# Performance work log

Measured on AMD Instinct MI355X. Metric: run time of the kernel, lower is better.

Reference implementation:

```python
import jax, jax.numpy as jnp
import numpy as np

MAX_DISP = 200


def conv2d(x, w, b):
    # x: [N,C,H,W], w: [O,I,3,3], stride 1, pad 1 == SAME
    y = jax.lax.conv_general_dilated(x, w, (1, 1), 'SAME',
                                     dimension_numbers=('NCHW', 'OIHW', 'NCHW'))
    return y + b[None, :, None, None]


def bn(x, g, b, m, v):
    # eval-mode BatchNorm2d with running stats (eps=1e-5)
    inv = jax.lax.rsqrt(v[None, :, None, None] + 1e-5)
    return g[None, :, None, None] * (x - m[None, :, None, None]) * inv + b[None, :, None, None]


def cost_volume(left, right, max_disp):
    # left, right: [c,h,w]. cost[d,y,x] = sum_c left[c,y,x] * padded[c,y,x+d]
    # where padded = [zeros(c,h,D), right] along w -- exact math of the torch loop.
    c, h, w = left.shape
    padded = jnp.concatenate([jnp.zeros((c, h, max_disp), left.dtype), right], axis=-1)

    def corr(d):
        win = jax.lax.dynamic_slice_in_dim(padded, d, w, axis=2)  # [c,h,w]
        return jnp.sum(left * win, axis=0)  # [h,w]

    return jax.vmap(corr)(jnp.arange(max_disp))  # [D,h,w]


def setup_inputs() -> dict:
    key = jax.random.key(0)
    ks = jax.random.split(key, 32)
    C, H, W = 32, 128, 256
    D = MAX_DISP
    inp = {}
    inp['left'] = jax.random.normal(ks[0], (1, C, H, W), jnp.float32)
    inp['right'] = jax.random.normal(ks[1], (1, C, H, W), jnp.float32)
    chans = [(64, D), (32, 64), (8, 32)]
    i = 2
    for idx, (co, ci) in enumerate(chans, 1):
        inp[f'w{idx}'] = jax.random.normal(ks[i], (co, ci, 3, 3), jnp.float32) * 0.05; i += 1
        inp[f'b{idx}'] = jax.random.normal(ks[i], (co,), jnp.float32) * 0.05; i += 1
        inp[f'g{idx}'] = 1.0 + 0.1 * jax.random.normal(ks[i], (co,), jnp.float32); i += 1
        inp[f'be{idx}'] = 0.1 * jax.random.normal(ks[i], (co,), jnp.float32); i += 1
        inp[f'm{idx}'] = 0.1 * jax.random.normal(ks[i], (co,), jnp.float32); i += 1
        inp[f'v{idx}'] = jax.random.uniform(ks[i], (co,), jnp.float32, minval=0.5, maxval=1.5); i += 1
    inp['w4'] = jax.random.normal(ks[i], (1, 8, 3, 3), jnp.float32) * 0.05; i += 1
    inp['b4'] = jax.random.normal(ks[i], (1,), jnp.float32) * 0.05
    return inp


def reference(left, right, w1, b1, g1, be1, m1, v1, w2, b2, g2, be2, m2, v2,
              w3, b3, g3, be3, m3, v3, w4, b4):
    vol = cost_volume(left[0], right[0], MAX_DISP)[None]  # [1, D, H, W]
    x = jax.nn.relu(bn(conv2d(vol, w1, b1), g1, be1, m1, v1))
    x = jax.nn.relu(bn(conv2d(x, w2, b2), g2, be2, m2, v2))
    x = jax.nn.relu(bn(conv2d(x, w3, b3), g3, be3, m3, v3))
    x = conv2d(x, w4, b4)
    return x[0]  # [1, H, W] (torch squeezes batch dim 0)
```

## Files before the change

### kernel.cpp

```cpp
#include <hip/hip_runtime.h>

#define HH 128
#define WW 256
#define CV_C 32
#define DISP 200

typedef __attribute__((ext_vector_type(4))) float f32x4;
typedef __attribute__((ext_vector_type(8))) short bf16x8;

__device__ inline unsigned short f2bf(float f) {
  unsigned int u = __float_as_uint(f);
  u = (u + 0x7FFFu + ((u >> 16) & 1u)) >> 16;
  return (unsigned short)u;
}

__device__ inline float bf2f(short s) {
  return __uint_as_float(((unsigned int)(unsigned short)s) << 16);
}

#define MAP_YX4()                                   \
  const int slot = bid >> 3;                        \
  const int y = ((bid & 7) << 4) + (slot & 15);     \
  const int x0 = (slot >> 4) << 6;

__global__ __launch_bounds__(256) void k1_cv_pack(
    const float* __restrict__ left, const float* __restrict__ right,
    const float* __restrict__ w1, const float* __restrict__ w2,
    const float* __restrict__ w3, unsigned short* __restrict__ pw1,
    unsigned short* __restrict__ pb2, unsigned short* __restrict__ pb3,
    unsigned short* __restrict__ cost_t) {
  __shared__ unsigned short r_sh[272][40];
  __shared__ unsigned short l_hi[64][40];
  __shared__ unsigned short l_lo[64][40];
  __shared__ unsigned short c_sh[64][224];
  const int bid = blockIdx.x;
  const int tid = threadIdx.x;

  if (bid >= 512) {
    const int b = bid - 512;
    if (b < 504) {
      const int idx = b * 256 + tid;
      const int j = idx & 7;
      const int n = (idx >> 3) & 63;
      const int kg = (idx >> 9) & 3;
      const int cp = idx >> 11;
      const int pos = cp % 9;
      const int chunk = cp / 9;
      const int ci = chunk * 32 + kg * 8 + j;
      float v = 0.f;
      if (ci < 200) v = w1[(n * 200 + ci) * 9 + pos];
      pw1[idx] = f2bf(v);
    } else if (b < 576) {
      const int idx = (b - 504) * 256 + tid;
      const int j = idx & 7;
      const int n = (idx >> 3) & 31;
      const int kg = (idx >> 8) & 3;
      const int kc = (idx >> 10) & 1;
      const int pos = idx >> 11;
      const int ci = kc * 32 + kg * 8 + j;
      pb2[idx] = f2bf(w2[(n * 64 + ci) * 9 + pos]);
    } else {
      const int idx = (b - 576) * 256 + tid;
      const int j = idx & 7;
      const int n = (idx >> 3) & 15;
      const int kg = (idx >> 7) & 3;
      const int pos = idx >> 9;
      const int ci = kg * 8 + j;
      float v = 0.f;
      if (n < 8) v = w3[(n * 32 + ci) * 9 + pos];
      pb3[idx] = f2bf(v);
    }
    return;
  }

  MAP_YX4();
  const int lane = tid & 63;
  const int wv = tid >> 6;
  const int col = lane & 15;
  const int kg = lane >> 4;

  for (int c = wv; c < CV_C; c += 4) {
    const float v = left[(c * HH + y) * WW + x0 + lane];
    const unsigned short h = f2bf(v);
    l_hi[lane][c] = h;
    l_lo[lane][c] = f2bf(v - bf2f(h));
  }
  for (int c = wv; c < CV_C; c += 4) {
    for (int pq = 0; pq < 320; pq += 64) {
      const int p = pq + lane;
      if (p < 272) {
        const int xp = x0 - 208 + p;
        float v = (xp >= 0) ? right[(c * HH + y) * WW + xp] : 0.f;
        r_sh[p][c] = f2bf(v);
      }
    }
  }
  {
    bf16x8 z = {0, 0, 0, 0, 0, 0, 0, 0};
    bf16x8* cz = (bf16x8*)c_sh;
#pragma unroll
    for (int k = 0; k < 7; ++k) cz[k * 256 + tid] = z;
  }
  __syncthreads();

  const bf16x8 b_hi = *(const bf16x8*)&l_hi[16 * wv + col][kg * 8];
  const bf16x8 b_lo = *(const bf16x8*)&l_lo[16 * wv + col][kg * 8];

  for (int t = 0; t < 14; ++t) {
    const int pq = 16 * (wv - t) + 208;
    const bf16x8 a_r = *(const bf16x8*)&r_sh[pq + col][kg * 8];
    f32x4 acc = {0.f, 0.f, 0.f, 0.f};
    acc = __builtin_amdgcn_mfma_f32_16x16x32_bf16(a_r, b_hi, acc, 0, 0, 0);
    acc = __builtin_amdgcn_mfma_f32_16x16x32_bf16(a_r, b_lo, acc, 0, 0, 0);
#pragma unroll
    for (int r = 0; r < 4; ++r) {
      const int d = 200 - 16 * t + kg * 4 + r - col;
      if (d >= 0 && d < DISP) c_sh[16 * wv + col][d] = f2bf(acc[r]);
    }
  }
  __syncthreads();

#pragma unroll
  for (int k = 0; k < 7; ++k) {
    const int s = k * 256 + tid;
    const int x = s / 28;
    const int dv = s - x * 28;
    *reinterpret_cast<bf16x8*>(&cost_t[(y * WW + x0 + x) * 224 + dv * 8]) =
        *reinterpret_cast<const bf16x8*>(&c_sh[x][dv * 8]);
  }
}

__global__ __launch_bounds__(256) void conv1_mfma_kernel(
    const unsigned short* __restrict__ cost_t,
    const unsigned short* __restrict__ pw,
    const float* __restrict__ bias, const float* __restrict__ gam,
    const float* __restrict__ bet, const float* __restrict__ mean,
    const float* __restrict__ var, unsigned short* __restrict__ out_t) {
  __shared__ unsigned short a_sh[2][3 * 66 * 40];
  const int bid = blockIdx.x;
  const int tid = threadIdx.x;
  MAP_YX4();
  const int lane = tid & 63;
  const int wv = tid >> 6;
  const int m0 = (wv >> 1) * 32;
  const int n0 = (wv & 1) * 32;
  const int col = lane & 15;
  const int kg = lane >> 4;

  long goff[4];
  int laddr[4];
  bool gvalid[4], lvalid[4];
#pragma unroll
  for (int it = 0; it < 4; ++it) {
    const int i = tid + it * 256;
    lvalid[it] = i < 792;
    const int row = i / 264;
    const int rem = i % 264;
    const int xx = rem >> 2;
    const int q = rem & 3;
    const int gy = y + row - 1;
    const int gx = x0 - 1 + xx;
    gvalid[it] = lvalid[it] && gy >= 0 && gy < HH && gx >= 0 && gx < WW;
    goff[it] = gvalid[it] ? (long)(gy * WW + gx) * 224 + q * 8 : 0;
    laddr[it] = (row * 66 + xx) * 40 + q * 8;
  }

  f32x4 acc[2][2];
#pragma unroll
  for (int i = 0; i < 2; ++i)
#pragma unroll
    for (int jx = 0; jx < 2; ++jx) acc[i][jx] = 0.f;

  const bf16x8* pwv = (const bf16x8*)pw;
  const bf16x8 zero = {0, 0, 0, 0, 0, 0, 0, 0};
  bf16x8 stg[4];

#pragma unroll
  for (int it = 0; it < 4; ++it)
    stg[it] = gvalid[it] ? *reinterpret_cast<const bf16x8*>(&cost_t[goff[it]])
                         : zero;
#pragma unroll
  for (int it = 0; it < 4; ++it)
    if (lvalid[it]) *reinterpret_cast<bf16x8*>(&a_sh[0][laddr[it]]) = stg[it];
  __syncthreads();

  for (int chunk = 0; chunk < 7; ++chunk) {
    const int buf = chunk & 1;
    if (chunk < 6) {
#pragma unroll
      for (int it = 0; it < 4; ++it)
        stg[it] = gvalid[it] ? *reinterpret_cast<const bf16x8*>(
                                   &cost_t[goff[it] + (chunk + 1) * 32])
                             : zero;
    }
    const bf16x8* av = (const bf16x8*)a_sh[buf];
#pragma unroll
    for (int pos = 0; pos < 9; ++pos) {
      const int ky = pos / 3;
      const int kx = pos % 3;
      const int bbase = ((chunk * 9 + pos) * 4 + kg) * 64;
      const bf16x8 b0v = pwv[bbase + n0 + col];
      const bf16x8 b1v = pwv[bbase + n0 + 16 + col];
      const bf16x8 a0v = av[(ky * 66 + m0 + col + kx) * 5 + kg];
      const bf16x8 a1v = av[(ky * 66 + m0 + 16 + col + kx) * 5 + kg];
      acc[0][0] = __builtin_amdgcn_mfma_f32_16x16x32_bf16(a0v, b0v, acc[0][0], 0, 0, 0);
      acc[0][1] = __builtin_amdgcn_mfma_f32_16x16x32_bf16(a0v, b1v, acc[0][1], 0, 0, 0);
      acc[1][0] = __builtin_amdgcn_mfma_f32_16x16x32_bf16(a1v, b0v, acc[1][0], 0, 0, 0);
      acc[1][1] = __builtin_amdgcn_mfma_f32_16x16x32_bf16(a1v, b1v, acc[1][1], 0, 0, 0);
    }
    if (chunk < 6) {
#pragma unroll
      for (int it = 0; it < 4; ++it)
        if (lvalid[it])
          *reinterpret_cast<bf16x8*>(&a_sh[buf ^ 1][laddr[it]]) = stg[it];
      __syncthreads();
    }
  }

#pragma unroll
  for (int nf = 0; nf < 2; ++nf) {
    const int c = n0 + nf * 16 + col;
    const float inv = rsqrtf(var[c] + 1e-5f);
    const float sc = gam[c] * inv;
    const float sh = bet[c] - mean[c] * sc;
    const float bb = bias[c];
#pragma unroll
    for (int mf = 0; mf < 2; ++mf) {
#pragma unroll
      for (int rr = 0; rr < 4; ++rr) {
        const int m = m0 + mf * 16 + kg * 4 + rr;
        float vv = (acc[mf][nf][rr] + bb) * sc + sh;
        vv = fmaxf(vv, 0.f);
        out_t[((y * WW + x0 + m) << 6) + c] = f2bf(vv);
      }
    }
  }
}

__global__ __launch_bounds__(256) void conv2_mfma_kernel(
    const unsigned short* __restrict__ in_t,
    const unsigned short* __restrict__ pb,
    const float* __restrict__ bias, const float* __restrict__ gam,
    const float* __restrict__ bet, const float* __restrict__ mean,
    const float* __restrict__ var, unsigned short* __restrict__ out_t) {
  __shared__ unsigned short a_sh[3 * 66 * 64];
  char* const ab = (char*)a_sh;
  const int bid = blockIdx.x;
  const int tid = threadIdx.x;
  MAP_YX4();
  const int lane = tid & 63;
  const int wv = tid >> 6;
  const int m0 = (wv >> 1) * 32;
  const int n0 = (wv & 1) * 16;
  const int col = lane & 15;
  const int kg = lane >> 4;

  f32x4 acc[2];
  acc[0] = 0.f;
  acc[1] = 0.f;

  for (int i = tid; i < 1584; i += 256) {
    const int r = i >> 3;
    const int q = i & 7;
    const int rowy = r / 66;
    const int xx = r % 66;
    const int gy = y + rowy - 1;
    const int gx = x0 - 1 + xx;
    bf16x8 v = {0, 0, 0, 0, 0, 0, 0, 0};
    if (gy >= 0 && gy < HH && gx >= 0 && gx < WW)
      v = *reinterpret_cast<const bf16x8*>(&in_t[((gy * WW + gx) << 6) + q * 8]);
    const int byte = ((r << 7) + (q << 4)) ^ ((r & 7) << 4);
    *reinterpret_cast<bf16x8*>(ab + byte) = v;
  }
  __syncthreads();

  const bf16x8* pbv = (const bf16x8*)pb;
#pragma unroll
  for (int pos = 0; pos < 9; ++pos) {
    const int ky = pos / 3;
    const int kx = pos % 3;
#pragma unroll
    for (int kc = 0; kc < 2; ++kc) {
      const bf16x8 bv = pbv[((pos * 2 + kc) * 4 + kg) * 32 + n0 + col];
#pragma unroll
      for (int mf = 0; mf < 2; ++mf) {
        const int r = ky * 66 + m0 + mf * 16 + col + kx;
        const int byte = ((r << 7) + (kc << 6) + (kg << 4)) ^ ((r & 7) << 4);
        const bf16x8 av = *reinterpret_cast<const bf16x8*>(ab + byte);
        acc[mf] = __builtin_amdgcn_mfma_f32_16x16x32_bf16(av, bv, acc[mf], 0, 0, 0);
      }
    }
  }

  const int c = n0 + col;
  const float inv = rsqrtf(var[c] + 1e-5f);
  const float sc = gam[c] * inv;
  const float sh = bet[c] - mean[c] * sc;
  const float bb = bias[c];
#pragma unroll
  for (int mf = 0; mf < 2; ++mf) {
#pragma unroll
    for (int rr = 0; rr < 4; ++rr) {
      const int m = m0 + mf * 16 + kg * 4 + rr;
      float vv = (acc[mf][rr] + bb) * sc + sh;
      vv = fmaxf(vv, 0.f);
      out_t[((y * WW + x0 + m) << 5) + c] = f2bf(vv);
    }
  }
}

__global__ __launch_bounds__(256) void conv3_mfma_kernel(
    const unsigned short* __restrict__ in_t,
    const unsigned short* __restrict__ pb,
    const float* __restrict__ bias, const float* __restrict__ gam,
    const float* __restrict__ bet, const float* __restrict__ mean,
    const float* __restrict__ var, unsigned short* __restrict__ out_t) {
  __shared__ unsigned short a_sh[3 * 66 * 32];
  char* const ab = (char*)a_sh;
  const int bid = blockIdx.x;
  const int tid = threadIdx.x;
  MAP_YX4();
  const int lane = tid & 63;
  const int wv = tid >> 6;
  const int m0 = wv * 16;
  const int col = lane & 15;
  const int kg = lane >> 4;

  f32x4 acc = 0.f;

  for (int i = tid; i < 792; i += 256) {
    const int r = i >> 2;
    const int q = i & 3;
    const int rowy = r / 66;
    const int xx = r % 66;
    const int gy = y + rowy - 1;
    const int gx = x0 - 1 + xx;
    bf16x8 v = {0, 0, 0, 0, 0, 0, 0, 0};
    if (gy >= 0 && gy < HH && gx >= 0 && gx < WW)
      v = *reinterpret_cast<const bf16x8*>(&in_t[((gy * WW + gx) << 5) + q * 8]);
    const int byte = ((r << 6) + (q << 4)) ^ ((r & 3) << 4);
    *reinterpret_cast<bf16x8*>(ab + byte) = v;
  }
  __syncthreads();

  const bf16x8* pbv = (const bf16x8*)pb;
#pragma unroll
  for (int pos = 0; pos < 9; ++pos) {
    const int ky = pos / 3;
    const int kx = pos % 3;
    const bf16x8 bv = pbv[(pos * 4 + kg) * 16 + col];
    const int r = ky * 66 + m0 + col + kx;
    const int byte = ((r << 6) + (kg << 4)) ^ ((r & 3) << 4);
    const bf16x8 av = *reinterpret_cast<const bf16x8*>(ab + byte);
    acc = __builtin_amdgcn_mfma_f32_16x16x32_bf16(av, bv, acc, 0, 0, 0);
  }

  if (col < 8) {
    const int c = col;
    const float inv = rsqrtf(var[c] + 1e-5f);
    const float sc = gam[c] * inv;
    const float sh = bet[c] - mean[c] * sc;
    const float bb = bias[c];
#pragma unroll
    for (int rr = 0; rr < 4; ++rr) {
      const int m = m0 + kg * 4 + rr;
      float vv = (acc[rr] + bb) * sc + sh;
      vv = fmaxf(vv, 0.f);
      out_t[((y * WW + x0 + m) << 3) + c] = f2bf(vv);
    }
  }
}

__global__ __launch_bounds__(256) void conv4_kernel(
    const unsigned short* __restrict__ in_t, const float* __restrict__ w4,
    const float* __restrict__ b4, float* __restrict__ out) {
  const int bid = blockIdx.x;
  const int y = ((bid & 7) << 4) + (bid >> 3);
  const int x = threadIdx.x;

  float wr[3][3][8];
#pragma unroll
  for (int ci = 0; ci < 8; ++ci)
#pragma unroll
    for (int ky = 0; ky < 3; ++ky)
#pragma unroll
      for (int kx = 0; kx < 3; ++kx) wr[ky][kx][ci] = w4[(ci * 3 + ky) * 3 + kx];

  float acc = b4[0];
#pragma unroll
  for (int ky = 0; ky < 3; ++ky) {
    const int gy = y + ky - 1;
    if (gy < 0 || gy >= HH) continue;
#pragma unroll
    for (int kx = 0; kx < 3; ++kx) {
      const int gx = x + kx - 1;
      if (gx < 0 || gx >= WW) continue;
      const bf16x8 v =
          *reinterpret_cast<const bf16x8*>(&in_t[((gy << 8) + gx) << 3]);
#pragma unroll
      for (int ci = 0; ci < 8; ++ci) acc += bf2f(v[ci]) * wr[ky][kx][ci];
    }
  }
  out[y * WW + x] = acc;
}

extern "C" void kernel_launch(void* const* d_in, const int* in_sizes, int n_in,
                              void* d_out, int out_size, void* d_ws,
                              size_t ws_size, hipStream_t stream) {
  const float* left = (const float*)d_in[0];
  const float* right = (const float*)d_in[1];
  const float* w1 = (const float*)d_in[2];
  const float* b1 = (const float*)d_in[3];
  const float* g1 = (const float*)d_in[4];
  const float* be1 = (const float*)d_in[5];
  const float* m1 = (const float*)d_in[6];
  const float* v1 = (const float*)d_in[7];
  const float* w2 = (const float*)d_in[8];
  const float* b2 = (const float*)d_in[9];
  const float* g2 = (const float*)d_in[10];
  const float* be2 = (const float*)d_in[11];
  const float* m2 = (const float*)d_in[12];
  const float* v2 = (const float*)d_in[13];
  const float* w3 = (const float*)d_in[14];
  const float* b3 = (const float*)d_in[15];
  const float* g3 = (const float*)d_in[16];
  const float* be3 = (const float*)d_in[17];
  const float* m3 = (const float*)d_in[18];
  const float* v3 = (const float*)d_in[19];
  const float* w4 = (const float*)d_in[20];
  const float* b4 = (const float*)d_in[21];

  char* ws = (char*)d_ws;
  unsigned short* cost_t = (unsigned short*)ws;
  char* region = ws + 14680064;
  unsigned short* pw1 = (unsigned short*)(region + 0);
  unsigned short* pb2 = (unsigned short*)(region + 262144);
  unsigned short* pb3 = (unsigned short*)(region + 327680);
  unsigned short* o1t = (unsigned short*)(region + 393216);
  unsigned short* o2t = (unsigned short*)(region + 4587520);
  unsigned short* o3t = (unsigned short*)(region + 6684672);
  float* o4 = (float*)d_out;

  k1_cv_pack<<<1106, 256, 0, stream>>>(left, right, w1, w2, w3, pw1, pb2, pb3,
                                       cost_t);
  conv1_mfma_kernel<<<512, 256, 0, stream>>>(cost_t, pw1, b1, g1, be1, m1, v1,
                                             o1t);
  conv2_mfma_kernel<<<512, 256, 0, stream>>>(o1t, pb2, b2, g2, be2, m2, v2,
                                             o2t);
  conv3_mfma_kernel<<<512, 256, 0, stream>>>(o2t, pb3, b3, g3, be3, m3, v3,
                                             o3t);
  conv4_kernel<<<128, 256, 0, stream>>>(o3t, w4, b4, o4);
}
```

Baseline: 51.40 us.

## Stage conv weight tiles in LDS instead of per-wave global loads

Measured after the change: 49.29 us. 4.1% less time.

```diff
diff --git a/kernel.cpp b/kernel.cpp
--- a/kernel.cpp
+++ b/kernel.cpp
@@ -136,7 +136,8 @@
     const float* __restrict__ bias, const float* __restrict__ gam,
     const float* __restrict__ bet, const float* __restrict__ mean,
     const float* __restrict__ var, unsigned short* __restrict__ out_t) {
-  __shared__ unsigned short a_sh[2][3 * 66 * 40];
+  __shared__ unsigned short a_sh[3 * 66 * 40];
+  __shared__ unsigned short b_sh[9 * 4 * 64 * 8];
   const int bid = blockIdx.x;
   const int tid = threadIdx.x;
   MAP_YX4();
@@ -172,35 +173,41 @@
     for (int jx = 0; jx < 2; ++jx) acc[i][jx] = 0.f;
 
   const bf16x8* pwv = (const bf16x8*)pw;
+  bf16x8* bsl = (bf16x8*)b_sh;
   const bf16x8 zero = {0, 0, 0, 0, 0, 0, 0, 0};
-  bf16x8 stg[4];
+  bf16x8 stgA[4], stgB[9];
 
 #pragma unroll
   for (int it = 0; it < 4; ++it)
-    stg[it] = gvalid[it] ? *reinterpret_cast<const bf16x8*>(&cost_t[goff[it]])
-                         : zero;
+    stgA[it] = gvalid[it] ? *reinterpret_cast<const bf16x8*>(&cost_t[goff[it]])
+                          : zero;
+#pragma unroll
+  for (int it = 0; it < 9; ++it) stgB[it] = pwv[tid + it * 256];
 #pragma unroll
   for (int it = 0; it < 4; ++it)
-    if (lvalid[it]) *reinterpret_cast<bf16x8*>(&a_sh[0][laddr[it]]) = stg[it];
+    if (lvalid[it]) *reinterpret_cast<bf16x8*>(&a_sh[laddr[it]]) = stgA[it];
+#pragma unroll
+  for (int it = 0; it < 9; ++it) bsl[tid + it * 256] = stgB[it];
   __syncthreads();
 
   for (int chunk = 0; chunk < 7; ++chunk) {
-    const int buf = chunk & 1;
     if (chunk < 6) {
 #pragma unroll
       for (int it = 0; it < 4; ++it)
-        stg[it] = gvalid[it] ? *reinterpret_cast<const bf16x8*>(
-                                   &cost_t[goff[it] + (chunk + 1) * 32])
-                             : zero;
-    }
-    const bf16x8* av = (const bf16x8*)a_sh[buf];
+        stgA[it] = gvalid[it] ? *reinterpret_cast<const bf16x8*>(
+                                    &cost_t[goff[it] + (chunk + 1) * 32])
+                              : zero;
+      const bf16x8* pwn = pwv + (chunk + 1) * 2304;
+#pragma unroll
+      for (int it = 0; it < 9; ++it) stgB[it] = pwn[tid + it * 256];
+    }
+    const bf16x8* av = (const bf16x8*)a_sh;
 #pragma unroll
     for (int pos = 0; pos < 9; ++pos) {
       const int ky = pos / 3;
       const int kx = pos % 3;
-      const int bbase = ((chunk * 9 + pos) * 4 + kg) * 64;
-      const bf16x8 b0v = pwv[bbase + n0 + col];
-      const bf16x8 b1v = pwv[bbase + n0 + 16 + col];
+      const bf16x8 b0v = bsl[(pos * 4 + kg) * 64 + n0 + col];
+      const bf16x8 b1v = bsl[(pos * 4 + kg) * 64 + n0 + 16 + col];
       const bf16x8 a0v = av[(ky * 66 + m0 + col + kx) * 5 + kg];
       const bf16x8 a1v = av[(ky * 66 + m0 + 16 + col + kx) * 5 + kg];
       acc[0][0] = __builtin_amdgcn_mfma_f32_16x16x32_bf16(a0v, b0v, acc[0][0], 0, 0, 0);
@@ -209,10 +216,12 @@
       acc[1][1] = __builtin_amdgcn_mfma_f32_16x16x32_bf16(a1v, b1v, acc[1][1], 0, 0, 0);
     }
     if (chunk < 6) {
+      __syncthreads();
 #pragma unroll
       for (int it = 0; it < 4; ++it)
-        if (lvalid[it])
-          *reinterpret_cast<bf16x8*>(&a_sh[buf ^ 1][laddr[it]]) = stg[it];
+        if (lvalid[it]) *reinterpret_cast<bf16x8*>(&a_sh[laddr[it]]) = stgA[it];
+#pragma unroll
+      for (int it = 0; it < 9; ++it) bsl[tid + it * 256] = stgB[it];
       __syncthreads();
     }
   }
@@ -244,6 +253,7 @@
     const float* __restrict__ bet, const float* __restrict__ mean,
     const float* __restrict__ var, unsigned short* __restrict__ out_t) {
   __shared__ unsigned short a_sh[3 * 66 * 64];
+  __shared__ unsigned short b_sh[18432];
   char* const ab = (char*)a_sh;
   const int bid = blockIdx.x;
   const int tid = threadIdx.x;
@@ -259,6 +269,12 @@
   acc[0] = 0.f;
   acc[1] = 0.f;
 
+  {
+    const bf16x8* pbv = (const bf16x8*)pb;
+    bf16x8* bsl = (bf16x8*)b_sh;
+#pragma unroll
+    for (int it = 0; it < 9; ++it) bsl[tid + it * 256] = pbv[tid + it * 256];
+  }
   for (int i = tid; i < 1584; i += 256) {
     const int r = i >> 3;
     const int q = i & 7;
@@ -274,14 +290,14 @@
   }
   __syncthreads();
 
-  const bf16x8* pbv = (const bf16x8*)pb;
+  const bf16x8* bsl = (const bf16x8*)b_sh;
 #pragma unroll
   for (int pos = 0; pos < 9; ++pos) {
     const int ky = pos / 3;
     const int kx = pos % 3;
 #pragma unroll
     for (int kc = 0; kc < 2; ++kc) {
-      const bf16x8 bv = pbv[((pos * 2 + kc) * 4 + kg) * 32 + n0 + col];
+      const bf16x8 bv = bsl[((pos * 2 + kc) * 4 + kg) * 32 + n0 + col];
 #pragma unroll
       for (int mf = 0; mf < 2; ++mf) {
         const int r = ky * 66 + m0 + mf * 16 + col + kx;
@@ -316,6 +332,7 @@
     const float* __restrict__ bet, const float* __restrict__ mean,
     const float* __restrict__ var, unsigned short* __restrict__ out_t) {
   __shared__ unsigned short a_sh[3 * 66 * 32];
+  __shared__ unsigned short b_sh[4608];
   char* const ab = (char*)a_sh;
   const int bid = blockIdx.x;
   const int tid = threadIdx.x;
@@ -328,6 +345,11 @@
 
   f32x4 acc = 0.f;
 
+  {
+    const bf16x8* pbv = (const bf16x8*)pb;
+    bf16x8* bsl = (bf16x8*)b_sh;
+    for (int s = tid; s < 576; s += 256) bsl[s] = pbv[s];
+  }
   for (int i = tid; i < 792; i += 256) {
     const int r = i >> 2;
     const int q = i & 3;
@@ -343,12 +365,12 @@
   }
   __syncthreads();
 
-  const bf16x8* pbv = (const bf16x8*)pb;
+  const bf16x8* bsl = (const bf16x8*)b_sh;
 #pragma unroll
   for (int pos = 0; pos < 9; ++pos) {
     const int ky = pos / 3;
     const int kx = pos % 3;
-    const bf16x8 bv = pbv[(pos * 4 + kg) * 16 + col];
+    const bf16x8 bv = bsl[(pos * 4 + kg) * 16 + col];
     const int r = ky * 66 + m0 + col + kx;
     const int byte = ((r << 6) + (kg << 4)) ^ ((r & 3) << 4);
     const bf16x8 av = *reinterpret_cast<const bf16x8*>(ab + byte);
```
